# Performance work log

Hardware: AMD Instinct MI355X
Metric: run time of the kernel (lower is better)

Reference implementation:

```python
import jax, jax.numpy as jnp
import numpy as np

N_NODES = 20000
N_EDGES = 160000
DIM = 64          # node embedding dim
SUB = 16          # sub_dim
NB = 5            # n_bonds_type
RB = 8            # radial basis size (FeNNol default)
CUTOFF = 5.0
NLAYERS = 3
HID = 64          # conv_hidden
NSPEC = 86        # species onehot size
XI_SHAPE = RB * SUB * NB   # 640
FC_IN = XI_SHAPE + SUB     # 656
LOG2 = float(np.log(2.0))


def ssp(x):
    # shifted softplus activation
    return jax.nn.softplus(x) - jnp.asarray(LOG2, x.dtype)


def radial_bessel(r):
    # sine Bessel radial basis on [0, cutoff]; r: [E] -> [E, RB]
    n = jnp.arange(1, RB + 1, dtype=r.dtype)
    x = r[:, None]
    return jnp.sqrt(jnp.asarray(2.0 / CUTOFF, r.dtype)) * jnp.sin(n * jnp.pi * x / CUTOFF) / x


def setup_inputs() -> dict:
    key = jax.random.key(0)
    ks = jax.random.split(key, 16)
    inp = {}
    inp['species'] = jax.random.randint(ks[0], (N_NODES,), 1, NSPEC, dtype=jnp.int32)
    inp['edge_src'] = jnp.sort(jax.random.randint(ks[1], (N_EDGES,), 0, N_NODES, dtype=jnp.int32))
    inp['edge_dst'] = jax.random.randint(ks[2], (N_EDGES,), 0, N_NODES, dtype=jnp.int32)
    # distances kept away from 0 to keep 1/r finite
    inp['distances'] = jax.random.uniform(ks[3], (N_EDGES,), jnp.float32, 0.5, CUTOFF)
    inp['switch'] = jax.random.uniform(ks[4], (N_EDGES,), jnp.float32)
    inp['bond_order'] = jax.random.uniform(ks[5], (N_EDGES, NB), jnp.float32)
    s = lambda fan: 1.0 / np.sqrt(fan)
    inp['W_species'] = jax.random.normal(ks[6], (NSPEC, DIM), jnp.float32) * s(NSPEC)
    inp['Wl'] = jax.random.normal(ks[7], (NLAYERS, DIM, 2 * SUB), jnp.float32) * s(DIM)
    inp['bl'] = jnp.zeros((NLAYERS, 2 * SUB), jnp.float32)
    inp['fcW1'] = jax.random.normal(ks[8], (NLAYERS, FC_IN, HID), jnp.float32) * s(FC_IN)
    inp['fcb1'] = jnp.zeros((NLAYERS, HID), jnp.float32)
    inp['fcW2'] = jax.random.normal(ks[9], (NLAYERS, HID, HID), jnp.float32) * s(HID)
    inp['fcb2'] = jnp.zeros((NLAYERS, HID), jnp.float32)
    inp['fcW3'] = jax.random.normal(ks[10], (NLAYERS, HID, DIM), jnp.float32) * s(HID)
    inp['fcb3'] = jnp.zeros((NLAYERS, DIM), jnp.float32)
    return inp


def reference(species, edge_src, edge_dst, distances, switch, bond_order,
              W_species, Wl, bl, fcW1, fcb1, fcW2, fcb2, fcW3, fcb3):
    # onehot(species) @ W (no bias) == embedding gather
    xi = W_species[species]                      # [N, DIM]
    rb = radial_bessel(distances)                # [E, RB]
    sw = switch[:, None]                         # [E, 1]
    for l in range(NLAYERS):
        h = xi @ Wl[l] + bl[l]                   # [N, 2*SUB]
        si, mi = h[:, :SUB], h[:, SUB:]
        # per-edge outer product: [E, RB, SUB, NB] -> [E, RB*SUB*NB]
        xi_j = (rb[:, :, None, None]
                * mi[edge_dst][:, None, :, None]
                * bond_order[:, None, None, :]).reshape(N_EDGES, XI_SHAPE)
        dxi = jax.ops.segment_sum(xi_j * sw, edge_src, num_segments=N_NODES)  # [N, 640]
        dxi = jnp.concatenate([dxi, si], axis=-1)                             # [N, 656]
        dxi = ssp(dxi @ fcW1[l] + fcb1[l])
        dxi = ssp(dxi @ fcW2[l] + fcb2[l])
        dxi = dxi @ fcW3[l] + fcb3[l]            # last FC layer linear
        xi = xi + dxi
    return xi
```

## Files before the change

kernel.cpp:

```cpp
#include <hip/hip_runtime.h>
#include <math.h>

#define N_NODES 20000
#define N_EDGES 160000
#define NTILES  1250

#define PI_F 3.14159265358979323846f
#define LN2_F 0.69314718055994530942f

#define W1PK 43008
#define W23PK 4096
#define WPK_LAYER 51200
#define WLPK_LAYER 2048
#define XROW 680
#define CAP 272
#define NFILL_MAX 232
#define WT_SLOTS 272
#define GSTRIDE 320

#define NW_XI   625
#define NW_PACK 616
#define NW_ROW  79
#define NW_TOTAL (NW_XI + NW_PACK + NW_ROW)

typedef short short8v __attribute__((ext_vector_type(8)));
typedef float f32x4 __attribute__((ext_vector_type(4)));
typedef unsigned short u16;
typedef unsigned long long ull;

__device__ __forceinline__ float sspf(float x) {
    return fmaxf(x, 0.0f) + log1pf(expf(-fabsf(x))) - LN2_F;
}
__device__ __forceinline__ u16 f2bf(float f) {
    unsigned int u = __float_as_uint(f);
    return (u16)((u + 0x7fffu + ((u >> 16) & 1u)) >> 16);
}
__device__ __forceinline__ unsigned int pk2(float a, float b) {
    return (unsigned int)f2bf(a) | ((unsigned int)f2bf(b) << 16);
}
__device__ __forceinline__ ull mge(int t) {
    t = t < 0 ? 0 : (t > 4 ? 4 : t);
    return t == 4 ? 0ULL : (~0ULL << (t * 16));
}


__device__ void row_start_work(int blk, const int* __restrict__ src,
                               int* __restrict__ row)
{
    int i = blk * 256 + threadIdx.x;
    if (i > N_NODES) return;
    int lo = 0, hi = N_EDGES;
    while (lo < hi) {
        int mid = (lo + hi) >> 1;
        if (src[mid] < i) lo = mid + 1; else hi = mid;
    }
    row[i] = lo;
}

__device__ void pack_w_work(int blk, const float* __restrict__ fcW1,
                            const float* __restrict__ fcW2,
                            const float* __restrict__ fcW3,
                            const float* __restrict__ Wl,
                            u16* __restrict__ Wpk,
                            u16* __restrict__ Wlpk)
{
    int idx = blk * 256 + threadIdx.x;
    if (idx >= 3 * WPK_LAYER + 2 * WLPK_LAYER) return;
    if (idx >= 3 * WPK_LAYER) {
        int r2 = idx - 3 * WPK_LAYER;
        int layer2 = r2 >> 11;
        int e = r2 & 2047;
        int j = e & 7, lane = (e >> 3) & 63;
        int rest = e >> 9;
        int ks = rest >> 1, cf = rest & 1;
        int k = ks * 32 + (lane >> 4) * 8 + j;
        int col = cf * 16 + (lane & 15);
        Wlpk[(size_t)layer2 * WLPK_LAYER + e] =
            f2bf(Wl[(size_t)(layer2 + 1) * 64 * 32 + (size_t)k * 32 + col]);
        return;
    }
    int layer = idx / WPK_LAYER;
    int r = idx - layer * WPK_LAYER;
    float val = 0.0f;
    if (r < W1PK) {
        int e = r;
        int j = e & 7, lane = (e >> 3) & 63, c16 = (e >> 9) & 3, ks = e >> 11;
        int k = ks * 32 + (lane >> 4) * 8 + j;
        int colm = c16 * 16 + (lane & 15);
        if (k < 640) {
            int nbv = k >> 4, ss = k & 15;
            int nn = nbv / 5, bb = nbv - nn * 5;
            val = fcW1[(size_t)layer * 656 * 64 + (size_t)(nn * 80 + ss * 5 + bb) * 64 + colm];
        } else if (k < 656) {
            val = fcW1[(size_t)layer * 656 * 64 + (size_t)k * 64 + colm];
        }
    } else {
        bool is2 = (r < W1PK + W23PK);
        const float* W = is2 ? fcW2 : fcW3;
        int e = is2 ? (r - W1PK) : (r - W1PK - W23PK);
        int j = e & 7, lane = (e >> 3) & 63, c16 = (e >> 9) & 3, ks = e >> 11;
        int k = ks * 32 + (lane >> 4) * 8 + j;
        int colm = c16 * 16 + (lane & 15);
        val = W[(size_t)layer * 64 * 64 + (size_t)k * 64 + colm];
    }
    Wpk[(size_t)layer * WPK_LAYER + r] = f2bf(val);
}

__device__ void xi_init_h_work(int blk, const int* __restrict__ species,
                               const float* __restrict__ Wsp,
                               const float* __restrict__ Wl0,
                               const float* __restrict__ bl0,
                               float* __restrict__ xi,
                               float* __restrict__ h, char* smem)
{
    float* xs = reinterpret_cast<float*>(smem);
    float* ws = reinterpret_cast<float*>(smem + 8192);
    int tid = threadIdx.x;
    int nb = blk * 32;

    #pragma unroll
    for (int i = 0; i < 2; ++i) {
        int idx = tid + i * 256;
        int node = idx >> 4, c4 = idx & 15;
        int sp = species[nb + node];
        float4 v = reinterpret_cast<const float4*>(Wsp + (size_t)sp * 64)[c4];
        reinterpret_cast<float4*>(xs)[idx] = v;
        reinterpret_cast<float4*>(xi)[(size_t)(nb + node) * 16 + c4] = v;
    }
    {
        const float4* wsrc = reinterpret_cast<const float4*>(Wl0);
        float4* wd = reinterpret_cast<float4*>(ws);
        #pragma unroll
        for (int i = 0; i < 2; ++i) wd[tid + i * 256] = wsrc[tid + i * 256];
    }
    __syncthreads();

    int c4g = tid & 7;
    int nrow = tid >> 3;
    float4 acc = *reinterpret_cast<const float4*>(bl0 + c4g * 4);
    const float* xr = xs + nrow * 64;
    #pragma unroll 8
    for (int j = 0; j < 64; ++j) {
        float xv = xr[j];
        float4 wv = *reinterpret_cast<const float4*>(ws + j * 32 + c4g * 4);
        acc.x = fmaf(xv, wv.x, acc.x);
        acc.y = fmaf(xv, wv.y, acc.y);
        acc.z = fmaf(xv, wv.z, acc.z);
        acc.w = fmaf(xv, wv.w, acc.w);
    }
    *reinterpret_cast<float4*>(h + (size_t)(nb + nrow) * 32 + c4g * 4) = acc;
}

__global__ __launch_bounds__(256) void setup_kernel(
    const int* __restrict__ species, const float* __restrict__ Wsp,
    const float* __restrict__ Wl, const float* __restrict__ bl0,
    float* __restrict__ xi, float* __restrict__ h0,
    const float* __restrict__ fcW1, const float* __restrict__ fcW2,
    const float* __restrict__ fcW3, u16* __restrict__ Wpk,
    u16* __restrict__ Wlpk,
    const int* __restrict__ esrc, int* __restrict__ rowp)
{
    __shared__ __align__(16) char smem[16384];
    int wk = blockIdx.x;
    if (wk < NW_XI)
        xi_init_h_work(wk, species, Wsp, Wl, bl0, xi, h0, smem);
    else if (wk < NW_XI + NW_PACK)
        pack_w_work(wk - NW_XI, fcW1, fcW2, fcW3, Wl, Wpk, Wlpk);
    else
        row_start_work(wk - NW_XI - NW_PACK, esrc, rowp);
}

__global__ __launch_bounds__(256) void agg_fc_fused(
    const float* __restrict__ dist,
    const float* __restrict__ sw,
    const float* __restrict__ bo,
    const int* __restrict__ row,
    const int* __restrict__ dst,
    const float* __restrict__ h_in,
    float* __restrict__ h_out,
    const u16* __restrict__ Wpk,
    const float* __restrict__ b1,
    const float* __restrict__ b2,
    const float* __restrict__ b3,
    const u16* __restrict__ Wlpk_l,
    const float* __restrict__ bl_next,
    int do_h,
    float* __restrict__ xi)
{
    __shared__ __align__(16) char smem[52224];
    u16 (*Xs)[XROW] = reinterpret_cast<u16(*)[XROW]>(smem);
    u16* wt  = reinterpret_cast<u16*>(smem + 21760);
    u16* mi  = reinterpret_cast<u16*>(smem + 43520);
    u16* Y1  = reinterpret_cast<u16*>(smem + 21760);
    u16* Y2  = reinterpret_cast<u16*>(smem + 21760 + 2304);
    float* Yo = reinterpret_cast<float*>(smem + 21760 + 4608);
    u16* Xnb  = reinterpret_cast<u16*>(smem + 8192);

    int tid = threadIdx.x;
    int wv = tid >> 6;
    int lane = tid & 63;
    int s = lane & 15;
    int kg = lane >> 4;
    int n0 = blockIdx.x * 16;
    int base = n0 + (wv << 2);

    int E0 = row[n0];
    int E1 = row[n0 + 16];
    int G0 = E0 & ~7;
    int nfill = E1 - G0;
    if (nfill > NFILL_MAX) nfill = NFILL_MAX;

    {
        int t = kg;
        u16* xr = &Xs[(wv << 2) + t][0];
        xr[640 + s] = f2bf(h_in[(size_t)(base + t) * 32 + s]);
        xr[656 + s] = 0;
    }

    for (int i = tid; i < WT_SLOTS; i += 256) {
        int e = G0 + i;
        u16* wcol = wt + (i >> 3) * GSTRIDE + (i & 7);
        if (i < nfill && e < N_EDGES) {
            float r = dist[e];
            float c = sqrtf(0.4f) / r * sw[e];
            float th = PI_F * r * 0.2f;
            float s1, c1v;
            __sincosf(th, &s1, &c1v);
            float k2c = 2.0f * c1v;
            float rbv[8];
            rbv[0] = s1;
            float sp = 0.0f, sc = s1;
            #pragma unroll
            for (int n = 1; n < 8; ++n) {
                float sn = k2c * sc - sp;
                rbv[n] = sn;
                sp = sc; sc = sn;
            }
            #pragma unroll
            for (int n = 0; n < 8; ++n) rbv[n] *= c;
            float bov[5];
            #pragma unroll
            for (int b = 0; b < 5; ++b) bov[b] = bo[(size_t)e * 5 + b];
            #pragma unroll
            for (int n = 0; n < 8; ++n)
                #pragma unroll
                for (int b = 0; b < 5; ++b)
                    wcol[(n * 5 + b) * 8] = f2bf(rbv[n] * bov[b]);
        } else {
            #pragma unroll
            for (int r2 = 0; r2 < 40; ++r2) wcol[r2 * 8] = 0;
        }
    }

    for (int i = tid; i < nfill; i += 256) {
        int d = dst[G0 + i];
        const float4* hp = reinterpret_cast<const float4*>(h_in + (size_t)d * 32 + 16);
        float4 v0 = hp[0], v1 = hp[1], v2 = hp[2], v3 = hp[3];
        u16* col = mi + i;
        col[0 * CAP]  = f2bf(v0.x); col[1 * CAP]  = f2bf(v0.y);
        col[2 * CAP]  = f2bf(v0.z); col[3 * CAP]  = f2bf(v0.w);
        col[4 * CAP]  = f2bf(v1.x); col[5 * CAP]  = f2bf(v1.y);
        col[6 * CAP]  = f2bf(v1.z); col[7 * CAP]  = f2bf(v1.w);
        col[8 * CAP]  = f2bf(v2.x); col[9 * CAP]  = f2bf(v2.y);
        col[10 * CAP] = f2bf(v2.z); col[11 * CAP] = f2bf(v2.w);
        col[12 * CAP] = f2bf(v3.x); col[13 * CAP] = f2bf(v3.y);
        col[14 * CAP] = f2bf(v3.z); col[15 * CAP] = f2bf(v3.w);
    }
    __syncthreads();

    for (int t = 0; t < 4; ++t) {
        int node = base + t;
        int e0 = row[node], e1 = row[node + 1];
        int e0a = e0 & ~7;
        int L0 = e0a - G0;
        int nks = (e1 - e0a + 31) >> 5;
        int maxks = (264 - L0) >> 5;
        if (nks > maxks) nks = maxks;

        f32x4 c0 = {0.f, 0.f, 0.f, 0.f};
        f32x4 c1 = {0.f, 0.f, 0.f, 0.f};
        f32x4 c2 = {0.f, 0.f, 0.f, 0.f};

        for (int kc = 0; kc < nks; ++kc) {
            int ebg = e0a + kc * 32 + kg * 8;
            int ebl = L0 + kc * 32 + kg * 8;
            uint4 bu = *reinterpret_cast<const uint4*>(mi + s * CAP + ebl);
            {
                int lo = e0 - ebg, hi = e1 - ebg;
                ull vA = mge(lo) & ~mge(hi);
                ull vB = mge(lo - 4) & ~mge(hi - 4);
                ull* bp = reinterpret_cast<ull*>(&bu);
                bp[0] &= vA;
                bp[1] &= vB;
            }
            short8v bfrag = *reinterpret_cast<short8v*>(&bu);
            const u16* gp = wt + (ebl >> 3) * GSTRIDE + s * 8;
            short8v a0 = *reinterpret_cast<const short8v*>(gp);
            short8v a1 = *reinterpret_cast<const short8v*>(gp + 128);
            short8v a2 = {0, 0, 0, 0, 0, 0, 0, 0};
            if (s < 8)
                a2 = *reinterpret_cast<const short8v*>(gp + 256);
            c0 = __builtin_amdgcn_mfma_f32_16x16x32_bf16(a0, bfrag, c0, 0, 0, 0);
            c1 = __builtin_amdgcn_mfma_f32_16x16x32_bf16(a1, bfrag, c1, 0, 0, 0);
            c2 = __builtin_amdgcn_mfma_f32_16x16x32_bf16(a2, bfrag, c2, 0, 0, 0);
        }

        u16* xr = &Xs[(wv << 2) + t][0];
        #pragma unroll
        for (int q = 0; q < 4; ++q) {
            xr[(kg * 4 + q) * 16 + s]      = f2bf(c0[q]);
            xr[(16 + kg * 4 + q) * 16 + s] = f2bf(c1[q]);
        }
        if (kg < 2) {
            #pragma unroll
            for (int q = 0; q < 4; ++q)
                xr[(32 + kg * 4 + q) * 16 + s] = f2bf(c2[q]);
        }
    }
    __syncthreads();

    int w = wv;
    int lrow = lane & 15;
    int lk = lane >> 4;
    int col = w * 16 + lrow;

    const u16* Wpk1 = Wpk;
    const u16* Wpk2 = Wpk + W1PK;
    const u16* Wpk3 = Wpk + W1PK + W23PK;

    f32x4 acc;
    {
        float bv = b1[col];
        acc[0] = bv; acc[1] = bv; acc[2] = bv; acc[3] = bv;
    }
    const u16* wp = Wpk1 + ((size_t)w * 64 + lane) * 8;
    #pragma unroll
    for (int ks = 0; ks < 21; ++ks) {
        short8v a = *reinterpret_cast<const short8v*>(&Xs[lrow][ks * 32 + lk * 8]);
        short8v b = *reinterpret_cast<const short8v*>(wp + (size_t)ks * 2048);
        acc = __builtin_amdgcn_mfma_f32_16x16x32_bf16(a, b, acc, 0, 0, 0);
    }
    __syncthreads();
    #pragma unroll
    for (int q = 0; q < 4; ++q)
        Y1[(lk * 4 + q) * 72 + col] = f2bf(sspf(acc[q]));
    __syncthreads();

    {
        float bv = b2[col];
        acc[0] = bv; acc[1] = bv; acc[2] = bv; acc[3] = bv;
    }
    #pragma unroll
    for (int ks = 0; ks < 2; ++ks) {
        short8v a = *reinterpret_cast<const short8v*>(&Y1[lrow * 72 + ks * 32 + lk * 8]);
        short8v b = *reinterpret_cast<const short8v*>(Wpk2 + ((size_t)(ks * 4 + w) * 64 + lane) * 8);
        acc = __builtin_amdgcn_mfma_f32_16x16x32_bf16(a, b, acc, 0, 0, 0);
    }
    __syncthreads();
    #pragma unroll
    for (int q = 0; q < 4; ++q)
        Y2[(lk * 4 + q) * 72 + col] = f2bf(sspf(acc[q]));
    __syncthreads();

    {
        float bv = b3[col];
        acc[0] = bv; acc[1] = bv; acc[2] = bv; acc[3] = bv;
    }
    #pragma unroll
    for (int ks = 0; ks < 2; ++ks) {
        short8v a = *reinterpret_cast<const short8v*>(&Y2[lrow * 72 + ks * 32 + lk * 8]);
        short8v b = *reinterpret_cast<const short8v*>(Wpk3 + ((size_t)(ks * 4 + w) * 64 + lane) * 8);
        acc = __builtin_amdgcn_mfma_f32_16x16x32_bf16(a, b, acc, 0, 0, 0);
    }
    #pragma unroll
    for (int q = 0; q < 4; ++q)
        Yo[(lk * 4 + q) * 68 + col] = acc[q];
    __syncthreads();

    {
        int rr = tid >> 4;
        int cc = tid & 15;
        float4 dv = *reinterpret_cast<const float4*>(Yo + rr * 68 + cc * 4);
        float4* xpn = reinterpret_cast<float4*>(xi + (size_t)(n0 + rr) * 64 + cc * 4);
        float4 o = *xpn;
        o.x += dv.x; o.y += dv.y; o.z += dv.z; o.w += dv.w;
        *xpn = o;
        if (do_h) {
            unsigned int* xb = reinterpret_cast<unsigned int*>(Xnb + rr * 64 + cc * 4);
            xb[0] = pk2(o.x, o.y);
            xb[1] = pk2(o.z, o.w);
        }
    }

    if (do_h) {
        __syncthreads();
        if (wv < 2) {
            int cf = wv;
            f32x4 hacc;
            {
                float bv = bl_next[cf * 16 + lrow];
                hacc[0] = bv; hacc[1] = bv; hacc[2] = bv; hacc[3] = bv;
            }
            #pragma unroll
            for (int ks = 0; ks < 2; ++ks) {
                short8v a = *reinterpret_cast<const short8v*>(
                    Xnb + lrow * 64 + ks * 32 + lk * 8);
                short8v b = *reinterpret_cast<const short8v*>(
                    Wlpk_l + ((size_t)(ks * 2 + cf) * 64 + lane) * 8);
                hacc = __builtin_amdgcn_mfma_f32_16x16x32_bf16(a, b, hacc, 0, 0, 0);
            }
            #pragma unroll
            for (int q = 0; q < 4; ++q)
                h_out[(size_t)(n0 + lk * 4 + q) * 32 + cf * 16 + lrow] = hacc[q];
        }
    }
}

extern "C" void kernel_launch(void* const* d_in, const int* in_sizes, int n_in,
                              void* d_out, int out_size, void* d_ws, size_t ws_size,
                              hipStream_t stream) {
    const int*   species = (const int*)d_in[0];
    const int*   esrc    = (const int*)d_in[1];
    const int*   edst    = (const int*)d_in[2];
    const float* dist    = (const float*)d_in[3];
    const float* sw      = (const float*)d_in[4];
    const float* bo      = (const float*)d_in[5];
    const float* Wsp     = (const float*)d_in[6];
    const float* Wl      = (const float*)d_in[7];
    const float* bl      = (const float*)d_in[8];
    const float* fcW1    = (const float*)d_in[9];
    const float* fcb1    = (const float*)d_in[10];
    const float* fcW2    = (const float*)d_in[11];
    const float* fcb2    = (const float*)d_in[12];
    const float* fcW3    = (const float*)d_in[13];
    const float* fcb3    = (const float*)d_in[14];
    float* xi = (float*)d_out;

    char* ws = (char*)d_ws;
    int*   rowp = (int*)ws;
    float* h0   = (float*)(ws + 80128);
    float* h1   = (float*)(ws + 2640128);
    u16*   Wpk  = (u16*)(ws + 5200128);
    u16*   Wlpk = (u16*)(ws + 5507328);

    hipLaunchKernelGGL(setup_kernel, dim3(NW_TOTAL), dim3(256), 0, stream,
                       species, Wsp, Wl, bl, xi, h0,
                       fcW1, fcW2, fcW3, Wpk, Wlpk,
                       esrc, rowp);

    float* hbuf[2] = {h0, h1};
    for (int l = 0; l < 3; ++l) {
        int do_h = (l < 2) ? 1 : 0;
        hipLaunchKernelGGL(agg_fc_fused, dim3(NTILES), dim3(256), 0, stream,
                           dist, sw, bo, rowp, edst,
                           hbuf[l & 1], hbuf[(l + 1) & 1],
                           Wpk + (size_t)l * WPK_LAYER,
                           fcb1 + (size_t)l * 64, fcb2 + (size_t)l * 64,
                           fcb3 + (size_t)l * 64,
                           Wlpk + (size_t)(do_h ? l : 0) * WLPK_LAYER,
                           bl + (size_t)(l + (do_h ? 1 : 0)) * 32,
                           do_h, xi);
    }
}
```

Baseline: 84.15 us.

## Cache per-edge radial-bond weights in global memory after layer zero

The first layer now computes the bf16 radial-basis times bond-order weight tile per edge group and also writes it to a global workspace buffer, zero-padding the tail. Layers one and two use a template variant that skips that computation and reads the A fragments straight from global memory. This drops the sincos, Chebyshev recurrence and bond-order loads from later layers and lowers their LDS footprint, which may raise occupancy. The cost is extra global traffic, about 12.8 MB written once and re-read from L2/HBM by the later layers, plus uncoalesced per-lane global loads inside the MFMA loop.

```diff
diff --git a/kernel.cpp b/kernel.cpp
--- a/kernel.cpp
+++ b/kernel.cpp
@@ -3,6 +3,9 @@
 
 #define N_NODES 20000
 #define N_EDGES 160000
+#define EPAD    160256
+#define NGROUPS (EPAD / 8)
+#define GSTRIDE 320
 #define NTILES  1250
 
 #define PI_F 3.14159265358979323846f
@@ -13,10 +16,7 @@
 #define WPK_LAYER 51200
 #define WLPK_LAYER 2048
 #define XROW 680
-#define CAP 272
-#define NFILL_MAX 232
 #define WT_SLOTS 272
-#define GSTRIDE 320
 
 #define NW_XI   625
 #define NW_PACK 616
@@ -170,10 +170,12 @@
         row_start_work(wk - NW_XI - NW_PACK, esrc, rowp);
 }
 
+template<int GENWT>
 __global__ __launch_bounds__(256) void agg_fc_fused(
     const float* __restrict__ dist,
     const float* __restrict__ sw,
     const float* __restrict__ bo,
+    u16* __restrict__ WTg,
     const int* __restrict__ row,
     const int* __restrict__ dst,
     const float* __restrict__ h_in,
@@ -187,10 +189,15 @@
     int do_h,
     float* __restrict__ xi)
 {
-    __shared__ __align__(16) char smem[52224];
+    constexpr int CAPv   = GENWT ? 272 : 312;
+    constexpr int NFILLv = GENWT ? 232 : 272;
+    constexpr int SMEMv  = GENWT ? 52224 : 31744;
+    constexpr int MIOFF  = GENWT ? 43520 : 21760;
+
+    __shared__ __align__(16) char smem[SMEMv];
     u16 (*Xs)[XROW] = reinterpret_cast<u16(*)[XROW]>(smem);
     u16* wt  = reinterpret_cast<u16*>(smem + 21760);
-    u16* mi  = reinterpret_cast<u16*>(smem + 43520);
+    u16* mi  = reinterpret_cast<u16*>(smem + MIOFF);
     u16* Y1  = reinterpret_cast<u16*>(smem + 21760);
     u16* Y2  = reinterpret_cast<u16*>(smem + 21760 + 2304);
     float* Yo = reinterpret_cast<float*>(smem + 21760 + 4608);
@@ -203,12 +210,15 @@
     int kg = lane >> 4;
     int n0 = blockIdx.x * 16;
     int base = n0 + (wv << 2);
+    int lrow = lane & 15;
+    int lk = lane >> 4;
+    int col = wv * 16 + lrow;
 
     int E0 = row[n0];
     int E1 = row[n0 + 16];
     int G0 = E0 & ~7;
     int nfill = E1 - G0;
-    if (nfill > NFILL_MAX) nfill = NFILL_MAX;
+    if (nfill > NFILLv) nfill = NFILLv;
 
     {
         int t = kg;
@@ -217,38 +227,43 @@
         xr[656 + s] = 0;
     }
 
-    for (int i = tid; i < WT_SLOTS; i += 256) {
-        int e = G0 + i;
-        u16* wcol = wt + (i >> 3) * GSTRIDE + (i & 7);
-        if (i < nfill && e < N_EDGES) {
-            float r = dist[e];
-            float c = sqrtf(0.4f) / r * sw[e];
-            float th = PI_F * r * 0.2f;
-            float s1, c1v;
-            __sincosf(th, &s1, &c1v);
-            float k2c = 2.0f * c1v;
-            float rbv[8];
-            rbv[0] = s1;
-            float sp = 0.0f, sc = s1;
-            #pragma unroll
-            for (int n = 1; n < 8; ++n) {
-                float sn = k2c * sc - sp;
-                rbv[n] = sn;
-                sp = sc; sc = sn;
+    if (GENWT) {
+        int G1 = (E1 + 7) & ~7;
+        int nW = G1 - G0;
+        if (nW > WT_SLOTS) nW = WT_SLOTS;
+        for (int i = tid; i < WT_SLOTS; i += 256) {
+            int e = G0 + i;
+            u16* wcol = wt + (i >> 3) * GSTRIDE + (i & 7);
+            if (i < nW && e < N_EDGES) {
+                float r = dist[e];
+                float c = sqrtf(0.4f) / r * sw[e];
+                float th = PI_F * r * 0.2f;
+                float s1, c1v;
+                __sincosf(th, &s1, &c1v);
+                float k2c = 2.0f * c1v;
+                float rbv[8];
+                rbv[0] = s1;
+                float sp = 0.0f, sc = s1;
+                #pragma unroll
+                for (int n = 1; n < 8; ++n) {
+                    float sn = k2c * sc - sp;
+                    rbv[n] = sn;
+                    sp = sc; sc = sn;
+                }
+                #pragma unroll
+                for (int n = 0; n < 8; ++n) rbv[n] *= c;
+                float bov[5];
+                #pragma unroll
+                for (int b = 0; b < 5; ++b) bov[b] = bo[(size_t)e * 5 + b];
+                #pragma unroll
+                for (int n = 0; n < 8; ++n)
+                    #pragma unroll
+                    for (int b = 0; b < 5; ++b)
+                        wcol[(n * 5 + b) * 8] = f2bf(rbv[n] * bov[b]);
+            } else {
+                #pragma unroll
+                for (int r2 = 0; r2 < 40; ++r2) wcol[r2 * 8] = 0;
             }
-            #pragma unroll
-            for (int n = 0; n < 8; ++n) rbv[n] *= c;
-            float bov[5];
-            #pragma unroll
-            for (int b = 0; b < 5; ++b) bov[b] = bo[(size_t)e * 5 + b];
-            #pragma unroll
-            for (int n = 0; n < 8; ++n)
-                #pragma unroll
-                for (int b = 0; b < 5; ++b)
-                    wcol[(n * 5 + b) * 8] = f2bf(rbv[n] * bov[b]);
-        } else {
-            #pragma unroll
-            for (int r2 = 0; r2 < 40; ++r2) wcol[r2 * 8] = 0;
         }
     }
 
@@ -256,17 +271,35 @@
         int d = dst[G0 + i];
         const float4* hp = reinterpret_cast<const float4*>(h_in + (size_t)d * 32 + 16);
         float4 v0 = hp[0], v1 = hp[1], v2 = hp[2], v3 = hp[3];
-        u16* col = mi + i;
-        col[0 * CAP]  = f2bf(v0.x); col[1 * CAP]  = f2bf(v0.y);
-        col[2 * CAP]  = f2bf(v0.z); col[3 * CAP]  = f2bf(v0.w);
-        col[4 * CAP]  = f2bf(v1.x); col[5 * CAP]  = f2bf(v1.y);
-        col[6 * CAP]  = f2bf(v1.z); col[7 * CAP]  = f2bf(v1.w);
-        col[8 * CAP]  = f2bf(v2.x); col[9 * CAP]  = f2bf(v2.y);
-        col[10 * CAP] = f2bf(v2.z); col[11 * CAP] = f2bf(v2.w);
-        col[12 * CAP] = f2bf(v3.x); col[13 * CAP] = f2bf(v3.y);
-        col[14 * CAP] = f2bf(v3.z); col[15 * CAP] = f2bf(v3.w);
-    }
-    __syncthreads();
+        u16* colp = mi + i;
+        colp[0 * CAPv]  = f2bf(v0.x); colp[1 * CAPv]  = f2bf(v0.y);
+        colp[2 * CAPv]  = f2bf(v0.z); colp[3 * CAPv]  = f2bf(v0.w);
+        colp[4 * CAPv]  = f2bf(v1.x); colp[5 * CAPv]  = f2bf(v1.y);
+        colp[6 * CAPv]  = f2bf(v1.z); colp[7 * CAPv]  = f2bf(v1.w);
+        colp[8 * CAPv]  = f2bf(v2.x); colp[9 * CAPv]  = f2bf(v2.y);
+        colp[10 * CAPv] = f2bf(v2.z); colp[11 * CAPv] = f2bf(v2.w);
+        colp[12 * CAPv] = f2bf(v3.x); colp[13 * CAPv] = f2bf(v3.y);
+        colp[14 * CAPv] = f2bf(v3.z); colp[15 * CAPv] = f2bf(v3.w);
+    }
+    __syncthreads();
+
+    if (GENWT) {
+        int G1 = (E1 + 7) & ~7;
+        int ngw = (G1 - G0) >> 3;
+        if (ngw > WT_SLOTS / 8) ngw = WT_SLOTS / 8;
+        for (int i = tid; i < ngw * 40; i += 256) {
+            int g = i / 40, rdw = i - g * 40;
+            uint4 v = *reinterpret_cast<const uint4*>(wt + g * GSTRIDE + rdw * 8);
+            *reinterpret_cast<uint4*>(
+                WTg + (size_t)((G0 >> 3) + g) * GSTRIDE + rdw * 8) = v;
+        }
+        if (blockIdx.x == NTILES - 1) {
+            uint4 z = make_uint4(0u, 0u, 0u, 0u);
+            for (int i = tid; i < (NGROUPS - N_EDGES / 8) * 40; i += 256)
+                *reinterpret_cast<uint4*>(
+                    WTg + (size_t)(N_EDGES / 8) * GSTRIDE + (size_t)i * 8) = z;
+        }
+    }
 
     for (int t = 0; t < 4; ++t) {
         int node = base + t;
@@ -274,8 +307,10 @@
         int e0a = e0 & ~7;
         int L0 = e0a - G0;
         int nks = (e1 - e0a + 31) >> 5;
-        int maxks = (264 - L0) >> 5;
-        if (nks > maxks) nks = maxks;
+        if (GENWT) {
+            int maxks = (264 - L0) >> 5;
+            if (nks > maxks) nks = maxks;
+        }
 
         f32x4 c0 = {0.f, 0.f, 0.f, 0.f};
         f32x4 c1 = {0.f, 0.f, 0.f, 0.f};
@@ -284,7 +319,7 @@
         for (int kc = 0; kc < nks; ++kc) {
             int ebg = e0a + kc * 32 + kg * 8;
             int ebl = L0 + kc * 32 + kg * 8;
-            uint4 bu = *reinterpret_cast<const uint4*>(mi + s * CAP + ebl);
+            uint4 bu = *reinterpret_cast<const uint4*>(mi + s * CAPv + ebl);
             {
                 int lo = e0 - ebg, hi = e1 - ebg;
                 ull vA = mge(lo) & ~mge(hi);
@@ -294,7 +329,9 @@
                 bp[1] &= vB;
             }
             short8v bfrag = *reinterpret_cast<short8v*>(&bu);
-            const u16* gp = wt + (ebl >> 3) * GSTRIDE + s * 8;
+            const u16* gp = GENWT
+                ? (wt + (ebl >> 3) * GSTRIDE + s * 8)
+                : (WTg + (size_t)(ebg >> 3) * GSTRIDE + (size_t)s * 8);
             short8v a0 = *reinterpret_cast<const short8v*>(gp);
             short8v a1 = *reinterpret_cast<const short8v*>(gp + 128);
             short8v a2 = {0, 0, 0, 0, 0, 0, 0, 0};
@@ -319,11 +356,6 @@
     }
     __syncthreads();
 
-    int w = wv;
-    int lrow = lane & 15;
-    int lk = lane >> 4;
-    int col = w * 16 + lrow;
-
     const u16* Wpk1 = Wpk;
     const u16* Wpk2 = Wpk + W1PK;
     const u16* Wpk3 = Wpk + W1PK + W23PK;
@@ -333,7 +365,7 @@
         float bv = b1[col];
         acc[0] = bv; acc[1] = bv; acc[2] = bv; acc[3] = bv;
     }
-    const u16* wp = Wpk1 + ((size_t)w * 64 + lane) * 8;
+    const u16* wp = Wpk1 + ((size_t)wv * 64 + lane) * 8;
     #pragma unroll
     for (int ks = 0; ks < 21; ++ks) {
         short8v a = *reinterpret_cast<const short8v*>(&Xs[lrow][ks * 32 + lk * 8]);
@@ -353,7 +385,7 @@
     #pragma unroll
     for (int ks = 0; ks < 2; ++ks) {
         short8v a = *reinterpret_cast<const short8v*>(&Y1[lrow * 72 + ks * 32 + lk * 8]);
-        short8v b = *reinterpret_cast<const short8v*>(Wpk2 + ((size_t)(ks * 4 + w) * 64 + lane) * 8);
+        short8v b = *reinterpret_cast<const short8v*>(Wpk2 + ((size_t)(ks * 4 + wv) * 64 + lane) * 8);
         acc = __builtin_amdgcn_mfma_f32_16x16x32_bf16(a, b, acc, 0, 0, 0);
     }
     __syncthreads();
@@ -369,7 +401,7 @@
     #pragma unroll
     for (int ks = 0; ks < 2; ++ks) {
         short8v a = *reinterpret_cast<const short8v*>(&Y2[lrow * 72 + ks * 32 + lk * 8]);
-        short8v b = *reinterpret_cast<const short8v*>(Wpk3 + ((size_t)(ks * 4 + w) * 64 + lane) * 8);
+        short8v b = *reinterpret_cast<const short8v*>(Wpk3 + ((size_t)(ks * 4 + wv) * 64 + lane) * 8);
         acc = __builtin_amdgcn_mfma_f32_16x16x32_bf16(a, b, acc, 0, 0, 0);
     }
     #pragma unroll
@@ -437,11 +469,12 @@
     float* xi = (float*)d_out;
 
     char* ws = (char*)d_ws;
-    int*   rowp = (int*)ws;
-    float* h0   = (float*)(ws + 80128);
-    float* h1   = (float*)(ws + 2640128);
-    u16*   Wpk  = (u16*)(ws + 5200128);
-    u16*   Wlpk = (u16*)(ws + 5507328);
+    u16*   WTg  = (u16*)ws;
+    int*   rowp = (int*)(ws + 12820480);
+    float* h0   = (float*)(ws + 12900608);
+    float* h1   = (float*)(ws + 15460608);
+    u16*   Wpk  = (u16*)(ws + 18020608);
+    u16*   Wlpk = (u16*)(ws + 18327808);
 
     hipLaunchKernelGGL(setup_kernel, dim3(NW_TOTAL), dim3(256), 0, stream,
                        species, Wsp, Wl, bl, xi, h0,
@@ -451,14 +484,25 @@
     float* hbuf[2] = {h0, h1};
     for (int l = 0; l < 3; ++l) {
         int do_h = (l < 2) ? 1 : 0;
-        hipLaunchKernelGGL(agg_fc_fused, dim3(NTILES), dim3(256), 0, stream,
-                           dist, sw, bo, rowp, edst,
-                           hbuf[l & 1], hbuf[(l + 1) & 1],
-                           Wpk + (size_t)l * WPK_LAYER,
-                           fcb1 + (size_t)l * 64, fcb2 + (size_t)l * 64,
-                           fcb3 + (size_t)l * 64,
-                           Wlpk + (size_t)(do_h ? l : 0) * WLPK_LAYER,
-                           bl + (size_t)(l + (do_h ? 1 : 0)) * 32,
-                           do_h, xi);
-    }
-}
+        if (l == 0) {
+            hipLaunchKernelGGL(HIP_KERNEL_NAME(agg_fc_fused<1>),
+                               dim3(NTILES), dim3(256), 0, stream,
+                               dist, sw, bo, WTg, rowp, edst,
+                               hbuf[0], hbuf[1],
+                               Wpk,
+                               fcb1, fcb2, fcb3,
+                               Wlpk, bl + 32, 1, xi);
+        } else {
+            hipLaunchKernelGGL(HIP_KERNEL_NAME(agg_fc_fused<0>),
+                               dim3(NTILES), dim3(256), 0, stream,
+                               dist, sw, bo, WTg, rowp, edst,
+                               hbuf[l & 1], hbuf[(l + 1) & 1],
+                               Wpk + (size_t)l * WPK_LAYER,
+                               fcb1 + (size_t)l * 64, fcb2 + (size_t)l * 64,
+                               fcb3 + (size_t)l * 64,
+                               Wlpk + (size_t)(do_h ? l : 0) * WLPK_LAYER,
+                               bl + (size_t)(l + (do_h ? 1 : 0)) * 32,
+                               do_h, xi);
+        }
+    }
+}
```

Result: faster. 82.33 us (-2.2%).
